# Kernel tuning notes

Hardware: AMD Instinct MI355X
Metric: run time of the kernel (lower is better)

Reference implementation:

```python
import jax, jax.numpy as jnp
import numpy as np

EPS = 1e-12  # matches torch F.normalize default eps


def _normalize(x):
    n = jnp.linalg.norm(x, axis=-1, keepdims=True)
    return x / jnp.maximum(n, EPS)


def _time_interp(t, e, L, E):
    """linear_interpolation_time: [B] t,e; L:[m] landmarks; E:[m,m] emb table."""
    m = L.shape[0]
    idx = jnp.searchsorted(L, t)              # torch.searchsorted, side='left'
    idx = jnp.where(idx == 0, 1, idx)
    idx = jnp.where(idx == m, m - 1, idx)
    E_hi, E_lo = E[idx], E[idx - 1]           # [B, m]
    L_hi, L_lo = L[idx], L[idx - 1]           # [B]
    coef = (E_hi - E_lo) / (L_hi - L_lo)[:, None]
    out = E_lo + coef * (t - L_lo)[:, None]
    # censor mask row i: mean of landmark embeddings j >= idx[i]
    denom = (m - idx).astype(E.dtype)[:, None]
    mask = (jnp.arange(m)[None, :] >= idx[:, None]).astype(E.dtype) / denom  # [B, m]
    out_censor = mask @ E.T                   # [B, m]
    e = e[:, None]
    return (out * e + out_censor * (1.0 - e)).astype(jnp.float32)


def setup_inputs() -> dict:
    key = jax.random.key(0)
    B, m = 8192, 256
    k_z, k_t, k_e = jax.random.split(key, 3)
    z = jax.random.normal(k_z, (B, m), dtype=jnp.float32)
    t = jax.random.uniform(k_t, (B,), dtype=jnp.float32, minval=0.0, maxval=10.0)
    e = (jax.random.uniform(k_e, (B,)) < 0.7).astype(jnp.float32)
    log_tau = jnp.zeros((1,), dtype=jnp.float32)            # tau=1.0 -> log 1 = 0
    time_landmark = jnp.linspace(0.0, 10.0, m, dtype=jnp.float32)
    time_emb_landmark = jnp.eye(m, dtype=jnp.float32)        # learnable eye init
    return {"z": z, "t": t, "e": e, "log_tau": log_tau,
            "time_emb_landmark": time_emb_landmark, "time_landmark": time_landmark}


def reference(z, t, e, log_tau, time_emb_landmark, time_landmark):
    B = z.shape[0]
    tau = jnp.sqrt(jnp.exp(log_tau))                         # [1]
    hz = _normalize(z) / tau                                  # enc = Identity
    hy = _normalize(_time_interp(t, e, time_landmark, time_emb_landmark)) / tau
    sim = hz @ hy.T                                           # [B, B]
    g = jnp.diagonal(sim)[:, None]                            # positives [B,1]
    # off-diagonal logits g0 - g: mask diagonal with -inf (exp -> 0 in logsumexp)
    eye = jnp.eye(B, dtype=bool)
    logits = jnp.where(eye, -jnp.inf, sim - g)
    slogits = jax.nn.logsumexp(logits, axis=1, keepdims=True)  # [B,1]
    # CrossEntropyLoss(sim, arange) per row = logsumexp(sim) - sim[i,i]
    dummy_ce = (jax.nn.logsumexp(sim, axis=1, keepdims=True) - g) - jnp.log(
        jnp.float32(B))
    out = jax.lax.stop_gradient(dummy_ce) + jnp.exp(
        slogits - jax.lax.stop_gradient(slogits)) - 1.0
    return jnp.clip(out, -5.0, 15.0)                          # [B,1]
```

## Files before the change

### kernel.cpp

```cpp
#include <hip/hip_runtime.h>
#include <hip/hip_bf16.h>

using short8  = __attribute__((ext_vector_type(8))) short;
using ushort8 = __attribute__((ext_vector_type(8))) unsigned short;
using f32x4   = __attribute__((ext_vector_type(4))) float;

__device__ inline void gload_lds16(const void* g, void* lds) {
    __builtin_amdgcn_global_load_lds(
        (const __attribute__((address_space(1))) void*)g,
        (__attribute__((address_space(3))) void*)lds, 16, 0, 0);
}

template <int CTRL>
__device__ inline float dpp_add(float x) {
    int v = __builtin_amdgcn_update_dpp(0, __float_as_int(x), CTRL, 0xf, 0xf, true);
    return x + __int_as_float(v);
}
__device__ inline float reduce16(float x) {
    x = dpp_add<0x121>(x);
    x = dpp_add<0x122>(x);
    x = dpp_add<0x124>(x);
    x = dpp_add<0x128>(x);
    return x;
}

__global__ __launch_bounds__(256) void suffix_kernel(const float* __restrict__ E,
                                                     float* __restrict__ ST, int m) {
    int j = blockIdx.x;
    int k = threadIdx.x;
    int lane = k & 63, w = k >> 6;
    __shared__ float wtot[4];
    float v = (k < m) ? E[(size_t)j * m + k] : 0.f;
    #pragma unroll
    for (int off = 1; off < 64; off <<= 1) {
        float o = __shfl_down(v, off);
        if (lane + off < 64) v += o;
    }
    if (lane == 0) wtot[w] = v;
    __syncthreads();
    float add = 0.f;
    #pragma unroll
    for (int w2 = 0; w2 < 4; ++w2)
        if (w2 > w) add += wtot[w2];
    v += add;
    if (k < m) ST[(size_t)k * m + j] = v;
}

__global__ __launch_bounds__(256) void prep_kernel(
    const float* __restrict__ z, const float* __restrict__ t,
    const float* __restrict__ e, const float* __restrict__ log_tau,
    const float* __restrict__ E, const float* __restrict__ L,
    const float* __restrict__ ST,
    __hip_bfloat16* __restrict__ hz, __hip_bfloat16* __restrict__ hy,
    float* __restrict__ g, float* __restrict__ acc, int B, int m)
{
    const int tid = threadIdx.x;
    const int row = blockIdx.x * 16 + (tid >> 4);
    const int sub = tid & 15;

    float tv = t[row], ev = e[row];

    int lo = 0, hi = m;
    while (lo < hi) { int mid = (lo + hi) >> 1; if (L[mid] < tv) lo = mid + 1; else hi = mid; }
    int idx = lo;
    if (idx == 0) idx = 1;
    if (idx == m) idx = m - 1;

    float Llo = L[idx - 1], Lhi = L[idx];
    float w    = (tv - Llo) / (Lhi - Llo);
    float invd = 1.0f / (float)(m - idx);
    float invtau = expf(-0.5f * log_tau[0]);

    const int j0 = sub * 16;
    f32x4 zv[4], El4[4], Eh4[4], Sc4[4], yv[4];
    #pragma unroll
    for (int q = 0; q < 4; ++q) {
        zv[q]  = *(const f32x4*)&z [(size_t)row * m + j0 + q * 4];
        El4[q] = *(const f32x4*)&E [(size_t)(idx - 1) * m + j0 + q * 4];
        Eh4[q] = *(const f32x4*)&E [(size_t)idx * m + j0 + q * 4];
        Sc4[q] = *(const f32x4*)&ST[(size_t)idx * m + j0 + q * 4];
    }
    float ssy = 0.f, ssz = 0.f;
    #pragma unroll
    for (int q = 0; q < 4; ++q)
        #pragma unroll
        for (int p = 0; p < 4; ++p) {
            float yint = El4[q][p] + (Eh4[q][p] - El4[q][p]) * w;
            float ycen = Sc4[q][p] * invd;
            float y = yint * ev + ycen * (1.f - ev);
            yv[q][p] = y; ssy += y * y;
            ssz += zv[q][p] * zv[q][p];
        }
    ssy = reduce16(ssy);
    ssz = reduce16(ssz);
    float sy = invtau / fmaxf(sqrtf(ssy), 1e-12f);
    float sz = invtau / fmaxf(sqrtf(ssz), 1e-12f);

    float gp = 0.f;
    ushort8 oy[2], oz[2];
    #pragma unroll
    for (int q = 0; q < 4; ++q)
        #pragma unroll
        for (int p = 0; p < 4; ++p) {
            float hyv = yv[q][p] * sy, hzv = zv[q][p] * sz;
            gp += hyv * hzv;
            __hip_bfloat16 hb = __float2bfloat16(hyv);
            __hip_bfloat16 zb = __float2bfloat16(hzv);
            oy[q >> 1][(q & 1) * 4 + p] = *reinterpret_cast<unsigned short*>(&hb);
            oz[q >> 1][(q & 1) * 4 + p] = *reinterpret_cast<unsigned short*>(&zb);
        }
    *(ushort8*)&hy[(size_t)row * m + j0]     = oy[0];
    *(ushort8*)&hy[(size_t)row * m + j0 + 8] = oy[1];
    *(ushort8*)&hz[(size_t)row * m + j0]     = oz[0];
    *(ushort8*)&hz[(size_t)row * m + j0 + 8] = oz[1];
    gp = reduce16(gp);
    if (sub == 0) { g[row] = gp; acc[row] = 0.f; }
}

__global__ __launch_bounds__(512, 2) void gemm_lse_kernel(
    const __hip_bfloat16* __restrict__ hz, const __hip_bfloat16* __restrict__ hy,
    float* __restrict__ row_acc, int Brows, int K)
{
    __shared__ __hip_bfloat16 As[4][256 * 32];
    __shared__ __hip_bfloat16 Bs[4][256 * 32];

    const int tid  = threadIdx.x;
    const int wid  = tid >> 6;
    const int lane = tid & 63;
    const int wm   = wid >> 2;
    const int wn   = wid & 3;
    const int lm   = lane & 15, lk = lane >> 4;

    int bx = blockIdx.x, by = blockIdx.y;
    if (gridDim.x == 32 && gridDim.y == 32) {
        int orig = by * 32 + bx;
        int xcd = orig & 7, pos = orig >> 3;
        by = (xcd << 2) | (pos & 3);
        bx = pos >> 2;
    }
    const int row0 = by * 256, col0 = bx * 256;

    f32x4 acc[8][4];
    #pragma unroll
    for (int i = 0; i < 8; ++i)
        #pragma unroll
        for (int j = 0; j < 4; ++j)
            acc[i][j] = (f32x4){0.f, 0.f, 0.f, 0.f};

#define FXOR(r) ((((r) & 3)) ^ (((r) >> 2) & 3))

    const int r0s = tid >> 2;
    const int q0  = (tid & 3) ^ FXOR(r0s);
    const int r1s = 128 + (tid >> 2);
    const int q1  = (tid & 3) ^ FXOR(r1s);
    const int ldsc0 = (wid * 64) * 8;
    const int ldsc1 = (512 + wid * 64) * 8;

#define STAGE_A(SB, kt)                                                           \
    do {                                                                          \
        gload_lds16(hz + (size_t)(row0 + r0s) * 256 + (kt) * 32 + q0 * 8,         \
                    (void*)&As[SB][ldsc0]);                                       \
        gload_lds16(hz + (size_t)(row0 + r1s) * 256 + (kt) * 32 + q1 * 8,         \
                    (void*)&As[SB][ldsc1]);                                       \
    } while (0)
#define STAGE_B(SB, kt)                                                           \
    do {                                                                          \
        gload_lds16(hy + (size_t)(col0 + r0s) * 256 + (kt) * 32 + q0 * 8,         \
                    (void*)&Bs[SB][ldsc0]);                                       \
        gload_lds16(hy + (size_t)(col0 + r1s) * 256 + (kt) * 32 + q1 * 8,         \
                    (void*)&Bs[SB][ldsc1]);                                       \
    } while (0)

    short8 a[4], b[4];
#define RD_A(BUF, H)                                                              \
    { _Pragma("unroll")                                                           \
      for (int mi = 0; mi < 4; ++mi) {                                            \
          int rt = wm * 128 + (H) * 64 + mi * 16 + lm;                            \
          a[mi] = *(const short8*)&As[BUF][rt * 32 + ((lk ^ FXOR(rt)) << 3)];     \
      } }
#define RD_B(BUF)                                                                 \
    { _Pragma("unroll")                                                           \
      for (int ni = 0; ni < 4; ++ni) {                                            \
          int rt = wn * 64 + ni * 16 + lm;                                        \
          b[ni] = *(const short8*)&Bs[BUF][rt * 32 + ((lk ^ FXOR(rt)) << 3)];     \
      } }
#define MM(BASE)                                                                  \
    { __builtin_amdgcn_s_setprio(1);                                              \
      _Pragma("unroll")                                                           \
      for (int mi = 0; mi < 4; ++mi)                                              \
          _Pragma("unroll")                                                       \
          for (int ni = 0; ni < 4; ++ni)                                          \
              acc[(BASE) + mi][ni] = __builtin_amdgcn_mfma_f32_16x16x32_bf16(     \
                  a[mi], b[ni], acc[(BASE) + mi][ni], 0, 0, 0);                   \
      __builtin_amdgcn_s_setprio(0); }

#define BAR do { asm volatile("" ::: "memory"); __builtin_amdgcn_s_barrier();     \
                 asm volatile("" ::: "memory"); } while (0)
#define WAITV(N) asm volatile("s_waitcnt vmcnt(" N ")" ::: "memory")

#define TILE(T, DO_STAGE, HAS_WAIT, WS)                                           \
    {                                                                             \
        RD_A((T) & 3, 0) RD_B((T) & 3)                                            \
        if (DO_STAGE) STAGE_A(((T) + 3) & 3, (T) + 3);                            \
        BAR;                                                                      \
        MM(0) BAR;                                                                \
        RD_A((T) & 3, 1)                                                          \
        if (DO_STAGE) STAGE_B(((T) + 3) & 3, (T) + 3);                            \
        if (HAS_WAIT) WAITV(WS);                                                  \
        BAR;                                                                      \
        MM(4) BAR;                                                                \
    }

    STAGE_A(0, 0); STAGE_B(0, 0);
    STAGE_A(1, 1); STAGE_B(1, 1);
    STAGE_A(2, 2); STAGE_B(2, 2);
    WAITV("8");
    BAR;

    TILE(0, 1, 1, "8")
    TILE(1, 1, 1, "8")
    TILE(2, 1, 1, "8")
    TILE(3, 1, 1, "8")
    TILE(4, 1, 1, "8")
    TILE(5, 0, 1, "4")
    TILE(6, 0, 1, "0")
    TILE(7, 0, 0, "0")

#undef TILE
#undef STAGE_A
#undef STAGE_B
#undef RD_A
#undef RD_B
#undef MM
#undef BAR
#undef WAITV
#undef FXOR

    const int lg = lane >> 4;
    #pragma unroll
    for (int mi = 0; mi < 8; ++mi) {
        float rs[4] = {0.f, 0.f, 0.f, 0.f};
        #pragma unroll
        for (int ni = 0; ni < 4; ++ni) {
            #pragma unroll
            for (int r = 0; r < 4; ++r) rs[r] += __expf(acc[mi][ni][r]);
        }
        #pragma unroll
        for (int r = 0; r < 4; ++r) {
            float s = reduce16(rs[r]);
            if (lm == 0)
                unsafeAtomicAdd(&row_acc[row0 + wm * 128 + mi * 16 + lg * 4 + r], s);
        }
    }
}

__global__ void finalize_kernel(const float* __restrict__ acc, const float* __restrict__ g,
                                float* __restrict__ out, int B) {
    int i = blockIdx.x * 256 + threadIdx.x;
    if (i < B) {
        float v = logf(acc[i]) - g[i] - logf((float)B);
        out[i] = fminf(fmaxf(v, -5.f), 15.f);
    }
}

extern "C" void kernel_launch(void* const* d_in, const int* in_sizes, int n_in,
                              void* d_out, int out_size, void* d_ws, size_t ws_size,
                              hipStream_t stream) {
    const float* z       = (const float*)d_in[0];
    const float* t       = (const float*)d_in[1];
    const float* e       = (const float*)d_in[2];
    const float* log_tau = (const float*)d_in[3];
    const float* E       = (const float*)d_in[4];
    const float* L       = (const float*)d_in[5];
    float* out = (float*)d_out;

    const int B = in_sizes[1];
    const int m = in_sizes[5];

    char* w = (char*)d_ws;
    __hip_bfloat16* hz = (__hip_bfloat16*)w;
    __hip_bfloat16* hy = hz + (size_t)B * m;
    float* ST   = (float*)(hy + (size_t)B * m);
    float* g    = ST + (size_t)m * m;
    float* acc  = g + B;

    suffix_kernel<<<m, 256, 0, stream>>>(E, ST, m);
    prep_kernel<<<B / 16, 256, 0, stream>>>(z, t, e, log_tau, E, L, ST, hz, hy, g, acc, B, m);
    dim3 grid2(32, 32);
    gemm_lse_kernel<<<grid2, 512, 0, stream>>>(hz, hy, acc, B, m);
    finalize_kernel<<<(B + 255) / 256, 256, 0, stream>>>(acc, g, out, B);
}
```

Baseline: 131.4 us.

## Shrink GEMM tile to 128x128 with 4 waves and 3-stage pipeline

The fused GEMM+logsumexp kernel moves from 256x256 tiles on 512 threads with a 4-deep LDS ring to 128x128 tiles on 256 threads with a 3-deep ring and one merged stage per k-step. The block swizzle over XCDs is redone for a 64x64 grid. Smaller blocks should raise occupancy (3 blocks per CU) and give 4096 blocks for better load balance. The cost is lower data reuse per tile, which doubles global/L2 traffic, and twice as many atomic adds into the row accumulators.

```diff
diff --git a/kernel.cpp b/kernel.cpp
--- a/kernel.cpp
+++ b/kernel.cpp
@@ -117,32 +117,32 @@
     if (sub == 0) { g[row] = gp; acc[row] = 0.f; }
 }
 
-__global__ __launch_bounds__(512, 2) void gemm_lse_kernel(
+__global__ __launch_bounds__(256, 3) void gemm_lse_kernel(
     const __hip_bfloat16* __restrict__ hz, const __hip_bfloat16* __restrict__ hy,
     float* __restrict__ row_acc, int Brows, int K)
 {
-    __shared__ __hip_bfloat16 As[4][256 * 32];
-    __shared__ __hip_bfloat16 Bs[4][256 * 32];
+    __shared__ __hip_bfloat16 As[3][128 * 32];
+    __shared__ __hip_bfloat16 Bs[3][128 * 32];
 
     const int tid  = threadIdx.x;
     const int wid  = tid >> 6;
     const int lane = tid & 63;
-    const int wm   = wid >> 2;
-    const int wn   = wid & 3;
+    const int wm   = wid >> 1;
+    const int wn   = wid & 1;
     const int lm   = lane & 15, lk = lane >> 4;
 
     int bx = blockIdx.x, by = blockIdx.y;
-    if (gridDim.x == 32 && gridDim.y == 32) {
-        int orig = by * 32 + bx;
+    if (gridDim.x == 64 && gridDim.y == 64) {
+        int orig = by * 64 + bx;
         int xcd = orig & 7, pos = orig >> 3;
-        by = (xcd << 2) | (pos & 3);
-        bx = pos >> 2;
-    }
-    const int row0 = by * 256, col0 = bx * 256;
-
-    f32x4 acc[8][4];
-    #pragma unroll
-    for (int i = 0; i < 8; ++i)
+        by = xcd * 8 + (pos >> 6);
+        bx = pos & 63;
+    }
+    const int row0 = by * 128, col0 = bx * 128;
+
+    f32x4 acc[4][4];
+    #pragma unroll
+    for (int i = 0; i < 4; ++i)
         #pragma unroll
         for (int j = 0; j < 4; ++j)
             acc[i][j] = (f32x4){0.f, 0.f, 0.f, 0.f};
@@ -151,20 +151,17 @@
 
     const int r0s = tid >> 2;
     const int q0  = (tid & 3) ^ FXOR(r0s);
-    const int r1s = 128 + (tid >> 2);
+    const int r1s = 64 + (tid >> 2);
     const int q1  = (tid & 3) ^ FXOR(r1s);
     const int ldsc0 = (wid * 64) * 8;
-    const int ldsc1 = (512 + wid * 64) * 8;
-
-#define STAGE_A(SB, kt)                                                           \
+    const int ldsc1 = (256 + wid * 64) * 8;
+
+#define STAGE(SB, kt)                                                             \
     do {                                                                          \
         gload_lds16(hz + (size_t)(row0 + r0s) * 256 + (kt) * 32 + q0 * 8,         \
                     (void*)&As[SB][ldsc0]);                                       \
         gload_lds16(hz + (size_t)(row0 + r1s) * 256 + (kt) * 32 + q1 * 8,         \
                     (void*)&As[SB][ldsc1]);                                       \
-    } while (0)
-#define STAGE_B(SB, kt)                                                           \
-    do {                                                                          \
         gload_lds16(hy + (size_t)(col0 + r0s) * 256 + (kt) * 32 + q0 * 8,         \
                     (void*)&Bs[SB][ldsc0]);                                       \
         gload_lds16(hy + (size_t)(col0 + r1s) * 256 + (kt) * 32 + q1 * 8,         \
@@ -172,65 +169,58 @@
     } while (0)
 
     short8 a[4], b[4];
-#define RD_A(BUF, H)                                                              \
+#define RD(BUF)                                                                   \
     { _Pragma("unroll")                                                           \
       for (int mi = 0; mi < 4; ++mi) {                                            \
-          int rt = wm * 128 + (H) * 64 + mi * 16 + lm;                            \
+          int rt = wm * 64 + mi * 16 + lm;                                        \
           a[mi] = *(const short8*)&As[BUF][rt * 32 + ((lk ^ FXOR(rt)) << 3)];     \
-      } }
-#define RD_B(BUF)                                                                 \
-    { _Pragma("unroll")                                                           \
+      }                                                                           \
+      _Pragma("unroll")                                                           \
       for (int ni = 0; ni < 4; ++ni) {                                            \
           int rt = wn * 64 + ni * 16 + lm;                                        \
           b[ni] = *(const short8*)&Bs[BUF][rt * 32 + ((lk ^ FXOR(rt)) << 3)];     \
       } }
-#define MM(BASE)                                                                  \
+#define MM                                                                        \
     { __builtin_amdgcn_s_setprio(1);                                              \
       _Pragma("unroll")                                                           \
       for (int mi = 0; mi < 4; ++mi)                                              \
           _Pragma("unroll")                                                       \
           for (int ni = 0; ni < 4; ++ni)                                          \
-              acc[(BASE) + mi][ni] = __builtin_amdgcn_mfma_f32_16x16x32_bf16(     \
-                  a[mi], b[ni], acc[(BASE) + mi][ni], 0, 0, 0);                   \
+              acc[mi][ni] = __builtin_amdgcn_mfma_f32_16x16x32_bf16(              \
+                  a[mi], b[ni], acc[mi][ni], 0, 0, 0);                            \
       __builtin_amdgcn_s_setprio(0); }
 
 #define BAR do { asm volatile("" ::: "memory"); __builtin_amdgcn_s_barrier();     \
                  asm volatile("" ::: "memory"); } while (0)
 #define WAITV(N) asm volatile("s_waitcnt vmcnt(" N ")" ::: "memory")
 
-#define TILE(T, DO_STAGE, HAS_WAIT, WS)                                           \
+#define TILE(T, SLOT, DO_STAGE, NSLOT, WS)                                        \
     {                                                                             \
-        RD_A((T) & 3, 0) RD_B((T) & 3)                                            \
-        if (DO_STAGE) STAGE_A(((T) + 3) & 3, (T) + 3);                            \
+        RD(SLOT)                                                                  \
+        if (DO_STAGE) STAGE(NSLOT, (T) + 2);                                      \
+        WAITV(WS);                                                                \
         BAR;                                                                      \
-        MM(0) BAR;                                                                \
-        RD_A((T) & 3, 1)                                                          \
-        if (DO_STAGE) STAGE_B(((T) + 3) & 3, (T) + 3);                            \
-        if (HAS_WAIT) WAITV(WS);                                                  \
+        MM                                                                        \
         BAR;                                                                      \
-        MM(4) BAR;                                                                \
-    }
-
-    STAGE_A(0, 0); STAGE_B(0, 0);
-    STAGE_A(1, 1); STAGE_B(1, 1);
-    STAGE_A(2, 2); STAGE_B(2, 2);
-    WAITV("8");
+    }
+
+    STAGE(0, 0);
+    STAGE(1, 1);
+    WAITV("4");
     BAR;
 
-    TILE(0, 1, 1, "8")
-    TILE(1, 1, 1, "8")
-    TILE(2, 1, 1, "8")
-    TILE(3, 1, 1, "8")
-    TILE(4, 1, 1, "8")
-    TILE(5, 0, 1, "4")
-    TILE(6, 0, 1, "0")
-    TILE(7, 0, 0, "0")
+    TILE(0, 0, 1, 2, "4")
+    TILE(1, 1, 1, 0, "4")
+    TILE(2, 2, 1, 1, "4")
+    TILE(3, 0, 1, 2, "4")
+    TILE(4, 1, 1, 0, "4")
+    TILE(5, 2, 1, 1, "4")
+    TILE(6, 0, 0, 0, "0")
+    TILE(7, 1, 0, 0, "0")
 
 #undef TILE
-#undef STAGE_A
-#undef STAGE_B
-#undef RD_A
-#undef RD_B
+#undef STAGE
+#undef RD
 #undef MM
 #undef BAR
 #undef WAITV
@@ -238,7 +228,7 @@
 
     const int lg = lane >> 4;
     #pragma unroll
-    for (int mi = 0; mi < 8; ++mi) {
+    for (int mi = 0; mi < 4; ++mi) {
         float rs[4] = {0.f, 0.f, 0.f, 0.f};
         #pragma unroll
         for (int ni = 0; ni < 4; ++ni) {
@@ -249,7 +239,7 @@
         for (int r = 0; r < 4; ++r) {
             float s = reduce16(rs[r]);
             if (lm == 0)
-                unsafeAtomicAdd(&row_acc[row0 + wm * 128 + mi * 16 + lg * 4 + r], s);
+                unsafeAtomicAdd(&row_acc[row0 + wm * 64 + mi * 16 + lg * 4 + r], s);
         }
     }
 }
@@ -286,7 +276,7 @@
 
     suffix_kernel<<<m, 256, 0, stream>>>(E, ST, m);
     prep_kernel<<<B / 16, 256, 0, stream>>>(z, t, e, log_tau, E, L, ST, hz, hy, g, acc, B, m);
-    dim3 grid2(32, 32);
-    gemm_lse_kernel<<<grid2, 512, 0, stream>>>(hz, hy, acc, B, m);
+    dim3 grid2(64, 64);
+    gemm_lse_kernel<<<grid2, 256, 0, stream>>>(hz, hy, acc, B, m);
     finalize_kernel<<<(B + 255) / 256, 256, 0, stream>>>(acc, g, out, B);
 }
```

Result: slower. 170.4 us (+29.7%).
